# Optimization experiments

Hardware: AMD Instinct MI355X
Metric: run time of the kernel (lower is better)

## Reference

```python
import jax, jax.numpy as jnp
import numpy as np

B, N, IN_FT, OUT_FT = 2, 4096, 512, 256
NEG = -9e15
EPS = 1e-12

def _prelu(x, a):
    return jnp.where(x >= 0, x, a * x)

def _normalize(x):
    n = jnp.sqrt(jnp.sum(x * x, axis=-1, keepdims=True))
    return x / jnp.maximum(n, EPS)

def _xavier(key, shape):
    fan_out, fan_in = shape
    lim = np.sqrt(6.0 / (fan_in + fan_out))
    return jax.random.uniform(key, shape, jnp.float32, -lim, lim)

def setup_inputs() -> dict:
    key = jax.random.key(0)
    ks = jax.random.split(key, 8)
    seq = jax.random.normal(ks[0], (B, N, IN_FT), jnp.float32)
    # sparse-ish random adjacency with self loops, row-normalized (typical GCN input)
    u = jax.random.uniform(ks[1], (B, N, N))
    mask = (u < 0.01).astype(jnp.float32)
    eye = jnp.eye(N, dtype=jnp.float32)[None]
    mask = jnp.maximum(mask, eye)
    adj = mask / jnp.sum(mask, axis=-1, keepdims=True)
    return {
        "seq": seq,
        "adj": adj,
        "W_fc": _xavier(ks[2], (OUT_FT, IN_FT)),
        "W_q": _xavier(ks[3], (OUT_FT, OUT_FT)),
        "W_k": _xavier(ks[4], (OUT_FT, OUT_FT)),
        "W_v1": _xavier(ks[5], (OUT_FT, OUT_FT)),
        "W_v2": _xavier(ks[6], (OUT_FT, OUT_FT)),
        "a_v": jnp.asarray(0.25, jnp.float32),    # PReLU inside to_v
        "a_act": jnp.asarray(0.25, jnp.float32),  # final PReLU self.act
        "bias": jnp.zeros((OUT_FT,), jnp.float32),
    }

def reference(seq, adj, W_fc, W_q, W_k, W_v1, W_v2, a_v, a_act, bias):
    # attn=True, training=False (dropout is identity) path of GCN.forward
    seq_fts = jnp.einsum('bnd,od->bno', seq, W_fc)            # fc (no bias)
    out = jnp.einsum('bmn,bno->bmo', adj, seq_fts)            # bmm(adj, seq_fts)
    out_q = _normalize(jnp.einsum('bno,po->bnp', out, W_q))
    out_k = _normalize(jnp.einsum('bno,po->bnp', out, W_k))
    attn_mx = jax.lax.stop_gradient(jnp.einsum('bmd,bnd->bmn', out_q, out_k))
    div_loss = jnp.mean(jnp.sum((out_q - out_k) ** 2, axis=-1))
    scores = jnp.where(adj > 0, attn_mx, NEG)
    attention = jax.nn.softmax(scores, axis=-1)               # dropout skipped (eval)
    ctx = jnp.einsum('bmn,bno->bmo', attention, out)
    h = _prelu(jnp.einsum('bno,po->bnp', ctx, W_v1), a_v)
    v = jnp.einsum('bno,po->bnp', h, W_v2)
    y = _prelu(v + bias, a_act)
    return (y, div_loss)
```

## Files before the change

kernel.cpp:

```cpp
#include <hip/hip_runtime.h>
#include <hip/hip_bf16.h>


#define NN    4096
#define ROWS  8192
#define OFT   256
#define CAP   128
#define NBLK  512
#define RPB   16
#define EPSN  1e-12f
#define MFMA(a,b,c) __builtin_amdgcn_mfma_f32_16x16x32_bf16((a),(b),(c),0,0,0)

typedef unsigned short ushort_t;
typedef __attribute__((ext_vector_type(8))) short bf16x8;
typedef __attribute__((ext_vector_type(4))) float f32x4;

#define WP_FC   0
#define WP_Q    (16384 * 8)
#define WP_K    (WP_Q + 8192 * 8)
#define WP_V1   (WP_K + 8192 * 8)
#define WP_V2   (WP_V1 + 8192 * 8)

__device__ __forceinline__ float lo_f(unsigned u) { union { unsigned i; float f; } c; c.i = u << 16;          return c.f; }
__device__ __forceinline__ float hi_f(unsigned u) { union { unsigned i; float f; } c; c.i = u & 0xFFFF0000u;  return c.f; }
__device__ __forceinline__ float bf2f(ushort_t u) { union { unsigned i; float f; } c; c.i = (unsigned)u << 16; return c.f; }
__device__ __forceinline__ ushort_t f2bf(float f) {
    union { float f; unsigned i; } c; c.f = f;
    unsigned r = c.i + 0x7FFFu + ((c.i >> 16) & 1u);
    return (ushort_t)(r >> 16);
}
__device__ __forceinline__ unsigned pack2(float a, float b) {
    return (unsigned)f2bf(a) | ((unsigned)f2bf(b) << 16);
}

__device__ __forceinline__ int detect32(const unsigned* w, int tid, int* scnt)
{
    if (tid == 0) *scnt = 0;
    __syncthreads();
    if (tid < 256) {
        union { unsigned i; float f; } c; c.i = w[tid];
        float a = fabsf(c.f);
        if (a > 1e-4f && a < 0.5f) atomicAdd(scnt, 1);
    }
    __syncthreads();
    return *scnt >= 128;
}

__global__ __launch_bounds__(256) void k0_prep(
    const void* __restrict__ Wfc, const void* __restrict__ Wq,
    const void* __restrict__ Wk,  const void* __restrict__ Wv1,
    const void* __restrict__ Wv2, ushort_t* __restrict__ Wp)
{
    __shared__ int scnt;
    const int tid = threadIdx.x;
    const int is32 = detect32((const unsigned*)Wfc, tid, &scnt);
    int sid = blockIdx.x * 256 + tid;
    const void* src; int K, local; ushort_t* dst;
    if (sid < 16384) { src = Wfc; K = 512; local = sid; dst = Wp + WP_FC + (size_t)local * 8; }
    else {
        int s = sid - 16384, which = s >> 13; local = s & 8191;
        const void* ws4[4] = {Wq, Wk, Wv1, Wv2};
        src = ws4[which]; K = 256;
        dst = Wp + WP_Q + (size_t)which * 65536 + (size_t)local * 8;
    }
    int col = local & 255, k8c = local >> 8;
    if (is32) {
        const float* p = (const float*)src + (size_t)col * K + k8c * 8;
        float4 x0 = *(const float4*)p, x1 = *(const float4*)(p + 4);
        uint4 o; o.x = pack2(x0.x, x0.y); o.y = pack2(x0.z, x0.w);
        o.z = pack2(x1.x, x1.y); o.w = pack2(x1.z, x1.w);
        *(uint4*)dst = o;
    } else {
        *(bf16x8*)dst = *(const bf16x8*)((const ushort_t*)src + (size_t)col * K + k8c * 8);
    }
}

__global__ __launch_bounds__(1024, 8) void k1_extract_fc(
    const void* __restrict__ seq, const void* __restrict__ adj,
    const void* __restrict__ Wfc, const ushort_t* __restrict__ Wp,
    ushort_t* __restrict__ regA, unsigned* __restrict__ gcv,
    int* __restrict__ cnt)
{
    __shared__ ushort_t Astage[64 * 17 * 8];
    __shared__ unsigned csr_cv[RPB * CAP];
    __shared__ int      csr_n[RPB];
    __shared__ int      scnt;

    const int tid = threadIdx.x, wave = tid >> 6, lane = tid & 63;
    const int t16 = lane & 15, kq = lane >> 4;
    const int b = blockIdx.x, r0 = b * RPB;

    const int is32 = detect32((const unsigned*)Wfc, tid, &scnt);

    {
        const int rl = wave;
        const size_t grow = (size_t)(r0 + rl);
        int base = 0;
        if (is32) {
            const float4* rowp = (const float4*)((const float*)adj + grow * NN);
            for (int h = 0; h < 4; ++h) {
                float4 v[4];
#pragma unroll
                for (int t = 0; t < 4; ++t) v[t] = rowp[(h * 4 + t) * 64 + lane];
                int c = 0;
#pragma unroll
                for (int t = 0; t < 4; ++t)
                    c += (v[t].x > 0.f) + (v[t].y > 0.f) + (v[t].z > 0.f) + (v[t].w > 0.f);
                int incl = c;
#pragma unroll
                for (int off = 1; off < 64; off <<= 1) {
                    int y = __shfl_up(incl, off, 64);
                    if (lane >= off) incl += y;
                }
                int p = base + incl - c;
                base += __shfl(incl, 63, 64);
#pragma unroll
                for (int t = 0; t < 4; ++t) {
                    float f[4] = {v[t].x, v[t].y, v[t].z, v[t].w};
#pragma unroll
                    for (int j = 0; j < 4; ++j)
                        if (f[j] > 0.f) {
                            if (p < CAP) {
                                unsigned col = ((h * 4 + t) * 64 + lane) * 4 + j;
                                csr_cv[rl * CAP + p] = (col << 16) | f2bf(f[j]);
                            }
                            ++p;
                        }
                }
            }
        } else {
            const uint2* rowp = (const uint2*)((const ushort_t*)adj + grow * NN);
            for (int h = 0; h < 4; ++h) {
                uint2 v[4];
#pragma unroll
                for (int t = 0; t < 4; ++t) v[t] = rowp[(h * 4 + t) * 64 + lane];
                int c = 0;
#pragma unroll
                for (int t = 0; t < 4; ++t)
                    c += (lo_f(v[t].x) > 0.f) + (hi_f(v[t].x) > 0.f)
                       + (lo_f(v[t].y) > 0.f) + (hi_f(v[t].y) > 0.f);
                int incl = c;
#pragma unroll
                for (int off = 1; off < 64; off <<= 1) {
                    int y = __shfl_up(incl, off, 64);
                    if (lane >= off) incl += y;
                }
                int p = base + incl - c;
                base += __shfl(incl, 63, 64);
#pragma unroll
                for (int t = 0; t < 4; ++t) {
                    ushort_t raw[4] = {(ushort_t)(v[t].x & 0xFFFF), (ushort_t)(v[t].x >> 16),
                                       (ushort_t)(v[t].y & 0xFFFF), (ushort_t)(v[t].y >> 16)};
#pragma unroll
                    for (int j = 0; j < 4; ++j)
                        if (bf2f(raw[j]) > 0.f) {
                            if (p < CAP) {
                                unsigned col = ((h * 4 + t) * 64 + lane) * 4 + j;
                                csr_cv[rl * CAP + p] = (col << 16) | raw[j];
                            }
                            ++p;
                        }
                }
            }
        }
        if (lane == 0) csr_n[rl] = (base < CAP) ? base : CAP;
    }
    __syncthreads();
    for (int i = tid; i < RPB * CAP; i += 1024)
        gcv[b * (RPB * CAP) + i] = csr_cv[i];
    if (tid < RPB) cnt[r0 + tid] = csr_n[tid];

    {
        int row = tid >> 6, seg = tid & 63;
        bf16x8 f0;
        if (is32) {
            const float* p = (const float*)seq + (size_t)(r0 + row) * 512 + seg * 8;
            float4 x0 = *(const float4*)p, x1 = *(const float4*)(p + 4);
            uint4 a;
            a.x = pack2(x0.x, x0.y); a.y = pack2(x0.z, x0.w);
            a.z = pack2(x1.x, x1.y); a.w = pack2(x1.z, x1.w);
            f0 = *(bf16x8*)&a;
        } else {
            f0 = *(const bf16x8*)((const ushort_t*)seq + (size_t)(r0 + row) * 512 + seg * 8);
        }
        *(bf16x8*)(Astage + ((size_t)seg * 17 + row) * 8) = f0;
    }
    __syncthreads();

    {
        const int col = wave * 16 + t16;
        const ushort_t* Wm = Wp + WP_FC;
        f32x4 a0 = {0.f, 0.f, 0.f, 0.f};
        for (int bch = 0; bch < 4; ++bch) {
            bf16x8 wb[4];
#pragma unroll
            for (int c2 = 0; c2 < 4; ++c2) {
                int k8c = (bch * 4 + c2) * 4 + kq;
                wb[c2] = *(const bf16x8*)(Wm + ((size_t)k8c * 256 + col) * 8);
            }
#pragma unroll
            for (int c2 = 0; c2 < 4; ++c2) {
                int c = bch * 4 + c2;
                bf16x8 af = *(const bf16x8*)(Astage + ((size_t)(c * 4 + kq) * 17 + t16) * 8);
                a0 = MFMA(af, wb[c2], a0);
            }
        }
#pragma unroll
        for (int r = 0; r < 4; ++r)
            regA[(size_t)(r0 + kq * 4 + r) * OFT + col] = f2bf(a0[r]);
    }
}

__global__ __launch_bounds__(512) void k2_spmm_qk(
    const ushort_t* __restrict__ regA, ushort_t* __restrict__ regKO,
    ushort_t* __restrict__ regQ, const ushort_t* __restrict__ Wp,
    const unsigned* __restrict__ gcv, const int* __restrict__ cnt,
    float* __restrict__ part)
{
    __shared__ ushort_t Astage[32 * 17 * 8];
    __shared__ unsigned csr_cv[RPB * CAP];
    __shared__ ushort_t qn_l[RPB * OFT];
    __shared__ float    red[2][RPB][4];
    __shared__ float    dlred[8];

    const int tid = threadIdx.x, wave = tid >> 6, lane = tid & 63;
    const int t16 = lane & 15, kq = lane >> 4;
    const int b = blockIdx.x, r0 = b * RPB;
    const size_t batb = (size_t)(b >> 8) * 4096;

    for (int i = tid; i < RPB * CAP; i += 512)
        csr_cv[i] = gcv[b * (RPB * CAP) + i];
    __syncthreads();

    {
        const int rA = wave * 2, rB = rA + 1;
        const int nA = cnt[r0 + rA], nB = cnt[r0 + rB];
        const int nm = max(nA, nB);
        const ushort_t* gA = regA + batb * OFT;
        float a0[4] = {0,0,0,0}, a1[4] = {0,0,0,0};
        unsigned cvA = 0, cvB = 0;
        uint2 uA = {0, 0}, uB = {0, 0};
        if (0 < nA) { cvA = csr_cv[rA*CAP]; uA = *(const uint2*)(gA + (size_t)(cvA >> 16) * OFT + lane * 4); }
        if (0 < nB) { cvB = csr_cv[rB*CAP]; uB = *(const uint2*)(gA + (size_t)(cvB >> 16) * OFT + lane * 4); }
        for (int i = 0; i < nm; ++i) {
            unsigned cvA1 = 0, cvB1 = 0;
            uint2 uA1 = {0, 0}, uB1 = {0, 0};
            if (i + 1 < nA) { cvA1 = csr_cv[rA*CAP + i + 1]; uA1 = *(const uint2*)(gA + (size_t)(cvA1 >> 16) * OFT + lane * 4); }
            if (i + 1 < nB) { cvB1 = csr_cv[rB*CAP + i + 1]; uB1 = *(const uint2*)(gA + (size_t)(cvB1 >> 16) * OFT + lane * 4); }
            if (i < nA) {
                float vv = bf2f((ushort_t)(cvA & 0xFFFF));
                a0[0]+=vv*lo_f(uA.x); a0[1]+=vv*hi_f(uA.x); a0[2]+=vv*lo_f(uA.y); a0[3]+=vv*hi_f(uA.y);
            }
            if (i < nB) {
                float vv = bf2f((ushort_t)(cvB & 0xFFFF));
                a1[0]+=vv*lo_f(uB.x); a1[1]+=vv*hi_f(uB.x); a1[2]+=vv*lo_f(uB.y); a1[3]+=vv*hi_f(uB.y);
            }
            cvA = cvA1; uA = uA1; cvB = cvB1; uB = uB1;
        }
        uint2 s0; s0.x = pack2(a0[0], a0[1]); s0.y = pack2(a0[2], a0[3]);
        uint2 s1; s1.x = pack2(a1[0], a1[1]); s1.y = pack2(a1[2], a1[3]);
        *(uint2*)(regKO + (size_t)(r0 + rA) * 512 + lane * 8 + 4) = s0;
        *(uint2*)(regKO + (size_t)(r0 + rB) * 512 + lane * 8 + 4) = s1;
        *(uint2*)(Astage + ((lane >> 1) * 17 + rA) * 8 + (lane & 1) * 4) = s0;
        *(uint2*)(Astage + ((lane >> 1) * 17 + rB) * 8 + (lane & 1) * 4) = s1;
    }
    __syncthreads();

    const int isK = wave >> 2, w4 = wave & 3;
    const ushort_t* Wm = Wp + (isK ? WP_K : WP_Q);
    f32x4 acc[4];
#pragma unroll
    for (int j = 0; j < 4; ++j) acc[j] = (f32x4){0.f,0.f,0.f,0.f};
    for (int bch = 0; bch < 4; ++bch) {
        bf16x8 wb[4][2];
#pragma unroll
        for (int j = 0; j < 4; ++j)
#pragma unroll
            for (int c2 = 0; c2 < 2; ++c2) {
                int col = w4 * 64 + j * 16 + t16;
                int k8c = (bch * 2 + c2) * 4 + kq;
                wb[j][c2] = *(const bf16x8*)(Wm + ((size_t)k8c * 256 + col) * 8);
            }
#pragma unroll
        for (int c2 = 0; c2 < 2; ++c2) {
            int c = bch * 2 + c2;
            bf16x8 af = *(const bf16x8*)(Astage + ((c*4 + kq) * 17 + t16) * 8);
#pragma unroll
            for (int j = 0; j < 4; ++j) acc[j] = MFMA(af, wb[j][c2], acc[j]);
        }
    }
#pragma unroll
    for (int r = 0; r < 4; ++r) {
        float s = 0.f;
#pragma unroll
        for (int j = 0; j < 4; ++j) s += acc[j][r] * acc[j][r];
#pragma unroll
        for (int off = 1; off < 16; off <<= 1) s += __shfl_xor(s, off, 16);
        if (t16 == 0) red[isK][kq*4 + r][w4] = s;
    }
    __syncthreads();
#pragma unroll
    for (int r = 0; r < 4; ++r) {
        int row = kq * 4 + r;
        float s = red[isK][row][0] + red[isK][row][1] + red[isK][row][2] + red[isK][row][3];
        float inv = 1.f / fmaxf(sqrtf(s), EPSN);
#pragma unroll
        for (int j = 0; j < 4; ++j) {
            int col = w4 * 64 + j * 16 + t16;
            float v = acc[j][r] * inv;
            acc[j][r] = v;
            ushort_t uv = f2bf(v);
            if (isK) regKO[(size_t)(r0 + row) * 512 + (col >> 2) * 8 + (col & 3)] = uv;
            else { qn_l[row * OFT + col] = uv; regQ[(size_t)(r0 + row) * OFT + col] = uv; }
        }
    }
    __syncthreads();
    if (isK) {
        float dl = 0.f;
#pragma unroll
        for (int r = 0; r < 4; ++r) {
            int row = kq * 4 + r;
#pragma unroll
            for (int j = 0; j < 4; ++j) {
                int col = w4 * 64 + j * 16 + t16;
                float d = bf2f(qn_l[row * OFT + col]) - acc[j][r];
                dl += d * d;
            }
        }
#pragma unroll
        for (int off = 1; off < 64; off <<= 1) dl += __shfl_xor(dl, off, 64);
        if (lane == 0) dlred[wave] = dl;
    }
    __syncthreads();
    if (tid == 0) part[b] = dlred[4] + dlred[5] + dlred[6] + dlred[7];
}

__global__ __launch_bounds__(512) void k3_attn_v(
    const ushort_t* __restrict__ regKO, const ushort_t* __restrict__ regQ,
    const unsigned* __restrict__ gcv, const int* __restrict__ cnt,
    const ushort_t* __restrict__ Wp, const void* __restrict__ Wfc,
    const void* __restrict__ a_v, const void* __restrict__ a_act,
    const void* __restrict__ biasv, const float* __restrict__ part,
    void* __restrict__ out)
{
    __shared__ ushort_t Astage[32 * 17 * 8];
    __shared__ ushort_t Hl[32 * 17 * 8];
    __shared__ unsigned csr_cv[RPB * CAP];
    __shared__ float    s8[8];
    __shared__ int      scnt;

    const int tid = threadIdx.x, wave = tid >> 6, lane = tid & 63;
    const int t16 = lane & 15, kq = lane >> 4;
    const int b = blockIdx.x, r0 = b * RPB;
    const size_t batb = (size_t)(b >> 8) * 4096;

    const int is32 = detect32((const unsigned*)Wfc, tid, &scnt);

    if (b == 0) {
        float s = part[tid];
#pragma unroll
        for (int off = 32; off; off >>= 1) s += __shfl_down(s, off, 64);
        if (lane == 0) s8[wave] = s;
        __syncthreads();
        if (tid == 0) {
            float t = s8[0]+s8[1]+s8[2]+s8[3]+s8[4]+s8[5]+s8[6]+s8[7];
            float v = t * (1.f / 8192.f);
            if (is32) ((float*)out)[(size_t)ROWS * OFT] = v;
            else      ((ushort_t*)out)[(size_t)ROWS * OFT] = f2bf(v);
        }
    }

    for (int i = tid; i < RPB * CAP; i += 512)
        csr_cv[i] = gcv[b * (RPB * CAP) + i];
    __syncthreads();

    {
        const int rA = wave * 2, rB = rA + 1;
        const int nA = cnt[r0 + rA], nB = cnt[r0 + rB];
        const int nm = max(nA, nB);
        uint2 qa = *(const uint2*)(regQ + (size_t)(r0 + rA) * OFT + lane * 4);
        uint2 qb = *(const uint2*)(regQ + (size_t)(r0 + rB) * OFT + lane * 4);
        float qA[4] = {lo_f(qa.x), hi_f(qa.x), lo_f(qa.y), hi_f(qa.y)};
        float qB[4] = {lo_f(qb.x), hi_f(qb.x), lo_f(qb.y), hi_f(qb.y)};
        const ushort_t* gKO = regKO + batb * 512;
        float sA = 0.f, sB = 0.f;
        float cA[4] = {0,0,0,0}, cB[4] = {0,0,0,0};
        uint4 vA = {0,0,0,0}, vB = {0,0,0,0};
        if (0 < nA) vA = *(const uint4*)(gKO + (size_t)(csr_cv[rA*CAP] >> 16) * 512 + lane * 8);
        if (0 < nB) vB = *(const uint4*)(gKO + (size_t)(csr_cv[rB*CAP] >> 16) * 512 + lane * 8);
        for (int i = 0; i < nm; ++i) {
            uint4 vA1 = {0,0,0,0}, vB1 = {0,0,0,0};
            if (i + 1 < nA) vA1 = *(const uint4*)(gKO + (size_t)(csr_cv[rA*CAP + i + 1] >> 16) * 512 + lane * 8);
            if (i + 1 < nB) vB1 = *(const uint4*)(gKO + (size_t)(csr_cv[rB*CAP + i + 1] >> 16) * 512 + lane * 8);
            if (i < nA) {
                float d = lo_f(vA.x)*qA[0] + hi_f(vA.x)*qA[1] + lo_f(vA.y)*qA[2] + hi_f(vA.y)*qA[3];
#pragma unroll
                for (int off = 1; off < 64; off <<= 1) d += __shfl_xor(d, off, 64);
                float es = __expf(d);
                sA += es;
                cA[0]+=es*lo_f(vA.z); cA[1]+=es*hi_f(vA.z); cA[2]+=es*lo_f(vA.w); cA[3]+=es*hi_f(vA.w);
            }
            if (i < nB) {
                float d = lo_f(vB.x)*qB[0] + hi_f(vB.x)*qB[1] + lo_f(vB.y)*qB[2] + hi_f(vB.y)*qB[3];
#pragma unroll
                for (int off = 1; off < 64; off <<= 1) d += __shfl_xor(d, off, 64);
                float es = __expf(d);
                sB += es;
                cB[0]+=es*lo_f(vB.z); cB[1]+=es*hi_f(vB.z); cB[2]+=es*lo_f(vB.w); cB[3]+=es*hi_f(vB.w);
            }
            vA = vA1; vB = vB1;
        }
        float iA = 1.f / sA, iB = 1.f / sB;
        uint2 s0; s0.x = pack2(cA[0]*iA, cA[1]*iA); s0.y = pack2(cA[2]*iA, cA[3]*iA);
        uint2 s1; s1.x = pack2(cB[0]*iB, cB[1]*iB); s1.y = pack2(cB[2]*iB, cB[3]*iB);
        *(uint2*)(Astage + ((lane >> 1) * 17 + rA) * 8 + (lane & 1) * 4) = s0;
        *(uint2*)(Astage + ((lane >> 1) * 17 + rB) * 8 + (lane & 1) * 4) = s1;
    }
    __syncthreads();

    const int col0 = wave * 32 + t16, col1 = col0 + 16;
    {
        const ushort_t* Wm = Wp + WP_V1;
        f32x4 h0 = {0.f,0.f,0.f,0.f}, h1 = {0.f,0.f,0.f,0.f};
        for (int bch = 0; bch < 2; ++bch) {
            bf16x8 wb0[4], wb1[4];
#pragma unroll
            for (int c2 = 0; c2 < 4; ++c2) {
                int k8c = (bch * 4 + c2) * 4 + kq;
                wb0[c2] = *(const bf16x8*)(Wm + ((size_t)k8c * 256 + col0) * 8);
                wb1[c2] = *(const bf16x8*)(Wm + ((size_t)k8c * 256 + col1) * 8);
            }
#pragma unroll
            for (int c2 = 0; c2 < 4; ++c2) {
                int c = bch * 4 + c2;
                bf16x8 af = *(const bf16x8*)(Astage + ((c*4 + kq) * 17 + t16) * 8);
                h0 = MFMA(af, wb0[c2], h0);
                h1 = MFMA(af, wb1[c2], h1);
            }
        }
        float av = is32 ? *(const float*)a_v : bf2f(*(const ushort_t*)a_v);
        int q0 = col0 >> 3, off0 = col0 & 7, q1 = col1 >> 3;
#pragma unroll
        for (int r = 0; r < 4; ++r) {
            int row = kq * 4 + r;
            float x0 = h0[r]; x0 = (x0 >= 0.f) ? x0 : av * x0;
            float x1 = h1[r]; x1 = (x1 >= 0.f) ? x1 : av * x1;
            Hl[(q0 * 17 + row) * 8 + off0] = f2bf(x0);
            Hl[(q1 * 17 + row) * 8 + off0] = f2bf(x1);
        }
    }
    __syncthreads();

    {
        const ushort_t* Wm = Wp + WP_V2;
        f32x4 y0 = {0.f,0.f,0.f,0.f}, y1 = {0.f,0.f,0.f,0.f};
        for (int bch = 0; bch < 2; ++bch) {
            bf16x8 wb0[4], wb1[4];
#pragma unroll
            for (int c2 = 0; c2 < 4; ++c2) {
                int k8c = (bch * 4 + c2) * 4 + kq;
                wb0[c2] = *(const bf16x8*)(Wm + ((size_t)k8c * 256 + col0) * 8);
                wb1[c2] = *(const bf16x8*)(Wm + ((size_t)k8c * 256 + col1) * 8);
            }
#pragma unroll
            for (int c2 = 0; c2 < 4; ++c2) {
                int c = bch * 4 + c2;
                bf16x8 af = *(const bf16x8*)(Hl + ((c*4 + kq) * 17 + t16) * 8);
                y0 = MFMA(af, wb0[c2], y0);
                y1 = MFMA(af, wb1[c2], y1);
            }
        }
        float aa = is32 ? *(const float*)a_act : bf2f(*(const ushort_t*)a_act);
        float bv0 = is32 ? ((const float*)biasv)[col0] : bf2f(((const ushort_t*)biasv)[col0]);
        float bv1 = is32 ? ((const float*)biasv)[col1] : bf2f(((const ushort_t*)biasv)[col1]);
#pragma unroll
        for (int r = 0; r < 4; ++r) {
            size_t row = (size_t)(r0 + kq * 4 + r);
            float x0 = y0[r] + bv0; x0 = (x0 >= 0.f) ? x0 : aa * x0;
            float x1 = y1[r] + bv1; x1 = (x1 >= 0.f) ? x1 : aa * x1;
            if (is32) {
                ((float*)out)[row * OFT + col0] = x0;
                ((float*)out)[row * OFT + col1] = x1;
            } else {
                ((ushort_t*)out)[row * OFT + col0] = f2bf(x0);
                ((ushort_t*)out)[row * OFT + col1] = f2bf(x1);
            }
        }
    }
}

extern "C" void kernel_launch(void* const* d_in, const int* in_sizes, int n_in,
                              void* d_out, int out_size, void* d_ws, size_t ws_size,
                              hipStream_t stream)
{
    const void* seq   = d_in[0];
    const void* adj   = d_in[1];
    const void* W_fc  = d_in[2];
    const void* W_q   = d_in[3];
    const void* W_k   = d_in[4];
    const void* W_v1  = d_in[5];
    const void* W_v2  = d_in[6];
    const void* a_v   = d_in[7];
    const void* a_act = d_in[8];
    const void* bias  = d_in[9];

    char* w = (char*)d_ws;
    ushort_t* regA  = (ushort_t*)w;
    ushort_t* regKO = (ushort_t*)(w + (4u  << 20));
    ushort_t* regQ  = (ushort_t*)(w + (12u << 20));
    unsigned* gcv   = (unsigned*)(w + (16u << 20));
    int*      cnt   = (int*)(w + (20u << 20));
    float*    part  = (float*)(w + (20u << 20) + 32768);
    ushort_t* Wp    = (ushort_t*)(w + (21u << 20));

    k0_prep<<<192, 256, 0, stream>>>(W_fc, W_q, W_k, W_v1, W_v2, Wp);
    k1_extract_fc<<<NBLK, 1024, 0, stream>>>(seq, adj, W_fc, Wp, regA, gcv, cnt);
    k2_spmm_qk<<<NBLK, 512, 0, stream>>>(regA, regKO, regQ, Wp, gcv, cnt, part);
    k3_attn_v<<<NBLK, 512, 0, stream>>>(regKO, regQ, gcv, cnt, Wp,
                                        W_fc, a_v, a_act, bias, part, d_out);
}
```

Before: 309.9 us.

## Split attention gather into separate kernel processing four neighbors per wave

The sparse attention/context stage moves out of the fused kernel into its own kernel that gives each wave one row (1024 blocks of 8 rows). Within a wave, four 16-lane groups handle four neighbors at once, and the dot-product reduction uses DPP row operations instead of a 6-step full-wave shuffle. This targets the latency-bound serial neighbor loop and its costly shuffle reductions. In exchange, it adds a kernel launch and a round trip of the context through global memory, reusing the regA workspace buffer.

```diff
diff --git a/kernel.cpp b/kernel.cpp
--- a/kernel.cpp
+++ b/kernel.cpp
@@ -31,6 +31,14 @@
 }
 __device__ __forceinline__ unsigned pack2(float a, float b) {
     return (unsigned)f2bf(a) | ((unsigned)f2bf(b) << 16);
+}
+
+template<int CTRL>
+__device__ __forceinline__ float dpp_add(float x) {
+    union { float f; int i; } c; c.f = x;
+    int y = __builtin_amdgcn_update_dpp(c.i, c.i, CTRL, 0xF, 0xF, false);
+    union { int i; float f; } r; r.i = y;
+    return x + r.f;
 }
 
 __device__ __forceinline__ int detect32(const unsigned* w, int tid, int* scnt)
@@ -335,24 +343,96 @@
     if (tid == 0) part[b] = dlred[4] + dlred[5] + dlred[6] + dlred[7];
 }
 
-__global__ __launch_bounds__(512) void k3_attn_v(
+__global__ __launch_bounds__(512) void k3a_attn(
     const ushort_t* __restrict__ regKO, const ushort_t* __restrict__ regQ,
-    const unsigned* __restrict__ gcv, const int* __restrict__ cnt,
-    const ushort_t* __restrict__ Wp, const void* __restrict__ Wfc,
-    const void* __restrict__ a_v, const void* __restrict__ a_act,
-    const void* __restrict__ biasv, const float* __restrict__ part,
-    void* __restrict__ out)
+    ushort_t* __restrict__ ctxG, const unsigned* __restrict__ gcv,
+    const int* __restrict__ cnt)
+{
+    __shared__ unsigned csr_cv[8 * CAP];
+    const int tid = threadIdx.x, wave = tid >> 6, lane = tid & 63;
+    const int t16 = lane & 15, grp = lane >> 4;
+    const int b = blockIdx.x, r0 = b * 8;
+    const size_t batb = (size_t)(b >> 9) * 4096;
+
+    for (int i = tid; i < 8 * CAP; i += 512)
+        csr_cv[i] = gcv[(size_t)r0 * CAP + i];
+    __syncthreads();
+
+    const int row = r0 + wave;
+    const int n = cnt[row];
+
+    float q[16];
+    {
+        const ushort_t* qp = regQ + (size_t)row * OFT + t16 * 16;
+        uint4 a = *(const uint4*)qp, bq = *(const uint4*)(qp + 8);
+        unsigned uu[8] = {a.x, a.y, a.z, a.w, bq.x, bq.y, bq.z, bq.w};
+#pragma unroll
+        for (int j = 0; j < 8; ++j) { q[2*j] = lo_f(uu[j]); q[2*j+1] = hi_f(uu[j]); }
+    }
+
+    const ushort_t* gKO = regKO + batb * 512;
+    float c[16];
+#pragma unroll
+    for (int j = 0; j < 16; ++j) c[j] = 0.f;
+    float sE = 0.f;
+
+    const int nIter = (n + 3) >> 2;
+    for (int it = 0; it < nIter; ++it) {
+        int e = it * 4 + grp;
+        int valid = (e < n);
+        unsigned cv = csr_cv[wave * CAP + (valid ? e : 0)];
+        const ushort_t* p = gKO + (size_t)(cv >> 16) * 512 + t16 * 32;
+        uint4 v[4];
+#pragma unroll
+        for (int i2 = 0; i2 < 4; ++i2) v[i2] = *(const uint4*)(p + i2 * 8);
+        float d = 0.f;
+#pragma unroll
+        for (int i2 = 0; i2 < 4; ++i2)
+            d += q[4*i2+0]*lo_f(v[i2].x) + q[4*i2+1]*hi_f(v[i2].x)
+               + q[4*i2+2]*lo_f(v[i2].y) + q[4*i2+3]*hi_f(v[i2].y);
+        d = dpp_add<0xB1>(d);
+        d = dpp_add<0x4E>(d);
+        d = dpp_add<0x124>(d);
+        d = dpp_add<0x128>(d);
+        float es = __expf(d);
+        es = valid ? es : 0.f;
+        sE += es;
+#pragma unroll
+        for (int i2 = 0; i2 < 4; ++i2) {
+            c[4*i2+0] += es * lo_f(v[i2].z); c[4*i2+1] += es * hi_f(v[i2].z);
+            c[4*i2+2] += es * lo_f(v[i2].w); c[4*i2+3] += es * hi_f(v[i2].w);
+        }
+    }
+#pragma unroll
+    for (int j = 0; j < 16; ++j) {
+        c[j] += __shfl_xor(c[j], 16, 64);
+        c[j] += __shfl_xor(c[j], 32, 64);
+    }
+    sE += __shfl_xor(sE, 16, 64);
+    sE += __shfl_xor(sE, 32, 64);
+    float inv = 1.f / sE;
+    {
+        int d0 = grp * 4;
+        uint2 st; st.x = pack2(c[d0]*inv, c[d0+1]*inv);
+        st.y = pack2(c[d0+2]*inv, c[d0+3]*inv);
+        *(uint2*)(ctxG + (size_t)row * OFT + t16 * 16 + d0) = st;
+    }
+}
+
+__global__ __launch_bounds__(512) void k3b_v(
+    const ushort_t* __restrict__ ctxG, const ushort_t* __restrict__ Wp,
+    const void* __restrict__ Wfc, const void* __restrict__ a_v,
+    const void* __restrict__ a_act, const void* __restrict__ biasv,
+    const float* __restrict__ part, void* __restrict__ out)
 {
     __shared__ ushort_t Astage[32 * 17 * 8];
     __shared__ ushort_t Hl[32 * 17 * 8];
-    __shared__ unsigned csr_cv[RPB * CAP];
     __shared__ float    s8[8];
     __shared__ int      scnt;
 
     const int tid = threadIdx.x, wave = tid >> 6, lane = tid & 63;
     const int t16 = lane & 15, kq = lane >> 4;
     const int b = blockIdx.x, r0 = b * RPB;
-    const size_t batb = (size_t)(b >> 8) * 4096;
 
     const int is32 = detect32((const unsigned*)Wfc, tid, &scnt);
 
@@ -370,51 +450,10 @@
         }
     }
 
-    for (int i = tid; i < RPB * CAP; i += 512)
-        csr_cv[i] = gcv[b * (RPB * CAP) + i];
-    __syncthreads();
-
-    {
-        const int rA = wave * 2, rB = rA + 1;
-        const int nA = cnt[r0 + rA], nB = cnt[r0 + rB];
-        const int nm = max(nA, nB);
-        uint2 qa = *(const uint2*)(regQ + (size_t)(r0 + rA) * OFT + lane * 4);
-        uint2 qb = *(const uint2*)(regQ + (size_t)(r0 + rB) * OFT + lane * 4);
-        float qA[4] = {lo_f(qa.x), hi_f(qa.x), lo_f(qa.y), hi_f(qa.y)};
-        float qB[4] = {lo_f(qb.x), hi_f(qb.x), lo_f(qb.y), hi_f(qb.y)};
-        const ushort_t* gKO = regKO + batb * 512;
-        float sA = 0.f, sB = 0.f;
-        float cA[4] = {0,0,0,0}, cB[4] = {0,0,0,0};
-        uint4 vA = {0,0,0,0}, vB = {0,0,0,0};
-        if (0 < nA) vA = *(const uint4*)(gKO + (size_t)(csr_cv[rA*CAP] >> 16) * 512 + lane * 8);
-        if (0 < nB) vB = *(const uint4*)(gKO + (size_t)(csr_cv[rB*CAP] >> 16) * 512 + lane * 8);
-        for (int i = 0; i < nm; ++i) {
-            uint4 vA1 = {0,0,0,0}, vB1 = {0,0,0,0};
-            if (i + 1 < nA) vA1 = *(const uint4*)(gKO + (size_t)(csr_cv[rA*CAP + i + 1] >> 16) * 512 + lane * 8);
-            if (i + 1 < nB) vB1 = *(const uint4*)(gKO + (size_t)(csr_cv[rB*CAP + i + 1] >> 16) * 512 + lane * 8);
-            if (i < nA) {
-                float d = lo_f(vA.x)*qA[0] + hi_f(vA.x)*qA[1] + lo_f(vA.y)*qA[2] + hi_f(vA.y)*qA[3];
-#pragma unroll
-                for (int off = 1; off < 64; off <<= 1) d += __shfl_xor(d, off, 64);
-                float es = __expf(d);
-                sA += es;
-                cA[0]+=es*lo_f(vA.z); cA[1]+=es*hi_f(vA.z); cA[2]+=es*lo_f(vA.w); cA[3]+=es*hi_f(vA.w);
-            }
-            if (i < nB) {
-                float d = lo_f(vB.x)*qB[0] + hi_f(vB.x)*qB[1] + lo_f(vB.y)*qB[2] + hi_f(vB.y)*qB[3];
-#pragma unroll
-                for (int off = 1; off < 64; off <<= 1) d += __shfl_xor(d, off, 64);
-                float es = __expf(d);
-                sB += es;
-                cB[0]+=es*lo_f(vB.z); cB[1]+=es*hi_f(vB.z); cB[2]+=es*lo_f(vB.w); cB[3]+=es*hi_f(vB.w);
-            }
-            vA = vA1; vB = vB1;
-        }
-        float iA = 1.f / sA, iB = 1.f / sB;
-        uint2 s0; s0.x = pack2(cA[0]*iA, cA[1]*iA); s0.y = pack2(cA[2]*iA, cA[3]*iA);
-        uint2 s1; s1.x = pack2(cB[0]*iB, cB[1]*iB); s1.y = pack2(cB[2]*iB, cB[3]*iB);
-        *(uint2*)(Astage + ((lane >> 1) * 17 + rA) * 8 + (lane & 1) * 4) = s0;
-        *(uint2*)(Astage + ((lane >> 1) * 17 + rB) * 8 + (lane & 1) * 4) = s1;
+    {
+        int row = tid >> 5, q0 = tid & 31;
+        bf16x8 f0 = *(const bf16x8*)(ctxG + (size_t)(r0 + row) * OFT + q0 * 8);
+        *(bf16x8*)(Astage + ((size_t)q0 * 17 + row) * 8) = f0;
     }
     __syncthreads();
 
@@ -516,6 +555,6 @@
     k0_prep<<<192, 256, 0, stream>>>(W_fc, W_q, W_k, W_v1, W_v2, Wp);
     k1_extract_fc<<<NBLK, 1024, 0, stream>>>(seq, adj, W_fc, Wp, regA, gcv, cnt);
     k2_spmm_qk<<<NBLK, 512, 0, stream>>>(regA, regKO, regQ, Wp, gcv, cnt, part);
-    k3_attn_v<<<NBLK, 512, 0, stream>>>(regKO, regQ, gcv, cnt, Wp,
-                                        W_fc, a_v, a_act, bias, part, d_out);
-}
+    k3a_attn<<<1024, 512, 0, stream>>>(regKO, regQ, regA, gcv, cnt);
+    k3b_v<<<NBLK, 512, 0, stream>>>(regA, Wp, W_fc, a_v, a_act, bias, part, d_out);
+}
```

Measured after the change: 296.1 us. 4.5% less time.
